# Kernel optimization log

Hardware: AMD Instinct MI355X
Metric: run time of the kernel (lower is better)

The kernel has to match this reference:

```python
import jax, jax.numpy as jnp
import numpy as np

N_NODES = 100000
N_EDGES = 640000
IN_C, HID_C, OUT_C = 128, 256, 128
N_GRAPHS = 64


def setup_inputs() -> dict:
    key = jax.random.key(0)
    k1, k2, k3, k4, k5, k6, k7 = jax.random.split(key, 7)
    x = jax.random.normal(k1, (N_NODES, IN_C), dtype=jnp.float32)
    edge_index = jax.random.randint(k2, (2, N_EDGES), 0, N_NODES, dtype=jnp.int32)
    batch = jnp.sort(jax.random.randint(k3, (N_NODES,), 0, N_GRAPHS, dtype=jnp.int32))
    s1 = 1.0 / np.sqrt(IN_C)
    s2 = 1.0 / np.sqrt(HID_C)
    W1 = jax.random.uniform(k4, (IN_C, HID_C), jnp.float32, -s1, s1)
    b1 = jax.random.uniform(k5, (HID_C,), jnp.float32, -s1, s1)
    W2 = jax.random.uniform(k6, (HID_C, OUT_C), jnp.float32, -s2, s2)
    b2 = jax.random.uniform(k7, (OUT_C,), jnp.float32, -s2, s2)
    return {"x": x, "edge_index": edge_index, "batch": batch,
            "W1": W1, "b1": b1, "W2": W2, "b2": b2}


def gcn_conv(x, src, dst, W, b, n_nodes):
    # GCNConv: D^{-1/2} (A + I) D^{-1/2} X W + b, degrees computed with self-loops
    ones = jnp.ones(src.shape[0], dtype=x.dtype)
    deg = jax.ops.segment_sum(ones, dst, num_segments=n_nodes) + 1.0  # self-loop
    inv_sqrt_deg = jax.lax.rsqrt(deg)
    h = x @ W  # [N, out]
    coef = inv_sqrt_deg[src] * inv_sqrt_deg[dst]  # [E]
    msgs = h[src] * coef[:, None]  # [E, out] -- dominant memory traffic
    agg = jax.ops.segment_sum(msgs, dst, num_segments=n_nodes)
    agg = agg + h * (inv_sqrt_deg * inv_sqrt_deg)[:, None]  # self-loop term
    return agg + b


def reference(x, edge_index, batch, W1, b1, W2, b2):
    n = x.shape[0]
    src, dst = edge_index[0], edge_index[1]
    h = jax.nn.relu(gcn_conv(x, src, dst, W1, b1, n))
    h = jax.nn.relu(gcn_conv(h, src, dst, W2, b2, n))
    # global mean pool over graphs
    sums = jax.ops.segment_sum(h, batch, num_segments=N_GRAPHS)
    counts = jax.ops.segment_sum(jnp.ones(n, dtype=h.dtype), batch, num_segments=N_GRAPHS)
    graph_embed = sums / jnp.maximum(counts, 1.0)[:, None]
    return h, graph_embed
```

## Files before the change

kernel.cpp:

```cpp
#include <hip/hip_runtime.h>

#define N_NODES  100000
#define N_EDGES  640000
#define IN_C     128
#define HID_C    256
#define OUT_C    128
#define N_GRAPHS 64
#define CAP      32

#define NBUK     256
#define NPB      ((N_NODES + NBUK - 1) / NBUK)
#define NSTRIPE  8
#define SCAP     448
#define BPB      (NSTRIPE * SCAP)
#define EPB      4096
#define EBLK     ((N_EDGES + EPB - 1) / EPB)

typedef _Float16 f16;
typedef _Float16 f16x4 __attribute__((ext_vector_type(4)));
typedef _Float16 f16x8 __attribute__((ext_vector_type(8)));
typedef float    f32x4 __attribute__((ext_vector_type(4)));


__global__ void zero_gcur_kernel(int* __restrict__ g) {
    int i = blockIdx.x * 256 + threadIdx.x;
    if (i < NBUK * NSTRIPE) g[i] = 0;
}


__global__ __launch_bounds__(256) void phaseA_kernel(
    const int* __restrict__ src, const int* __restrict__ dst,
    int* __restrict__ gcur, int* __restrict__ buckets,
    const float* __restrict__ x, f16* __restrict__ xh,
    const float* __restrict__ W1, f16* __restrict__ Wt1,
    const float* __restrict__ W2, f16* __restrict__ Wt2,
    int* __restrict__ gs) {
    int b = blockIdx.x;
    if (b < EBLK) {
        __shared__ int bcnt[NBUK];
        __shared__ int bbase[NBUK];
        int tid = threadIdx.x;
        int st  = b & (NSTRIPE - 1);
        for (int i = tid; i < NBUK; i += 256) bcnt[i] = 0;
        __syncthreads();
        int e0 = b * EPB + tid * 16;
        bool act = e0 < N_EDGES;
        int bk[16], pp[16], val[16];
        #pragma unroll
        for (int c = 0; c < 4; ++c) {
            int e = e0 + c * 4;
            int4 dq = act ? *reinterpret_cast<const int4*>(&dst[e]) : make_int4(0,0,0,0);
            int4 sq = act ? *reinterpret_cast<const int4*>(&src[e]) : make_int4(0,0,0,0);
            int dv[4] = {dq.x, dq.y, dq.z, dq.w};
            int sv[4] = {sq.x, sq.y, sq.z, sq.w};
            #pragma unroll
            for (int j = 0; j < 4; ++j) {
                int k = c * 4 + j;
                int bkj = (unsigned)dv[j] / NPB;
                bk[k]  = bkj;
                val[k] = ((dv[j] - bkj * NPB) << 17) | sv[j];
            }
        }
        #pragma unroll
        for (int k = 0; k < 16; ++k)
            pp[k] = act ? atomicAdd(&bcnt[bk[k]], 1) : 0;
        __syncthreads();
        if (tid < NBUK) {
            int c = bcnt[tid];
            if (c > 0) bbase[tid] = atomicAdd(&gcur[tid * NSTRIPE + st], c);
        }
        __syncthreads();
        if (act) {
            #pragma unroll
            for (int k = 0; k < 16; ++k) {
                int idx = bbase[bk[k]] + pp[k];
                if (idx < SCAP)
                    buckets[(size_t)bk[k] * BPB + st * SCAP + idx] = val[k];
            }
        }
        return;
    }
    b -= EBLK;
    if (b < 6250) {
        int i = (b * 256 + threadIdx.x) * 8;
        float4 a = *reinterpret_cast<const float4*>(&x[i]);
        float4 c = *reinterpret_cast<const float4*>(&x[i + 4]);
        f16x8 o = { (f16)a.x, (f16)a.y, (f16)a.z, (f16)a.w,
                    (f16)c.x, (f16)c.y, (f16)c.z, (f16)c.w };
        *reinterpret_cast<f16x8*>(&xh[i]) = o;
        return;
    }
    b -= 6250;
    if (b < 128) {
        int idx = b * 256 + threadIdx.x;
        int k = idx / HID_C, n = idx % HID_C;
        Wt1[n * IN_C + k] = (f16)W1[idx];
        return;
    }
    b -= 128;
    if (b < 128) {
        int idx = b * 256 + threadIdx.x;
        int k = idx / OUT_C, n = idx % OUT_C;
        Wt2[n * HID_C + k] = (f16)W2[idx];
        return;
    }
    if (threadIdx.x <= N_GRAPHS) gs[threadIdx.x] = N_NODES;
}
#define PHASEA_BLOCKS (EBLK + 6250 + 128 + 128 + 1)


__global__ __launch_bounds__(256) void phaseB_kernel(
    const int* __restrict__ gcur, const int* __restrict__ buckets,
    int2* __restrict__ meta, int* __restrict__ slots, float* __restrict__ isd,
    const int* __restrict__ batch, int* __restrict__ gs) {
    int b = blockIdx.x;
    if (b < NBUK) {
        __shared__ int cur[NPB];
        int tid = threadIdx.x;
        int v0 = b * NPB;
        int nv = min(NPB, N_NODES - v0);
        for (int i = tid; i < NPB; i += 256) cur[i] = 0;
        __syncthreads();
        for (int s = 0; s < NSTRIPE; ++s) {
            int n = min(gcur[b * NSTRIPE + s], SCAP);
            const int* seg = &buckets[(size_t)b * BPB + s * SCAP];
            for (int i = tid; i < n; i += 256) {
                int e = seg[i];
                int r = e >> 17;
                int pos = atomicAdd(&cur[r], 1);
                if (pos < CAP) slots[(size_t)(v0 + r) * CAP + pos] = e & 0x1FFFF;
            }
        }
        __syncthreads();
        for (int i = tid; i < nv; i += 256) {
            int c = cur[i];
            float iv = rsqrtf((float)c + 1.0f);
            meta[v0 + i] = make_int2(c, __float_as_int(iv));
            isd[v0 + i] = iv;
        }
        return;
    }
    b -= NBUK;
    int i = b * 256 + threadIdx.x;
    if (i < N_NODES) {
        int bt = batch[i];
        int pb = (i == 0) ? -1 : batch[i - 1];
        for (int g = pb + 1; g <= bt; ++g) gs[g] = i;
    }
}
#define PHASEB_BLOCKS (NBUK + (N_NODES + 255) / 256)


__global__ __launch_bounds__(512, 4) void gemm_fused_kernel(
    const f16* __restrict__ A,
    const f16* __restrict__ Wt1,
    const f16* __restrict__ Wt2,
    const float* __restrict__ b1,
    const float* __restrict__ isd,
    f16* __restrict__ T2, int M) {
    __shared__ f16 Wl[128 * 132];
    __shared__ f16 bounce[8][2][16 * 40];
    int tid  = threadIdx.x;
    int wid  = tid >> 6;
    int lane = tid & 63;
    int l16  = lane & 15;
    int kgrp = lane >> 4;
    int rowbase = blockIdx.x * 128 + wid * 16;
    int arow = rowbase + l16;
    bool okrow = arow < M;

    f16x8 a1[4];
    f16x8 zero = {};
    #pragma unroll
    for (int s = 0; s < 4; ++s)
        a1[s] = okrow ? *reinterpret_cast<const f16x8*>(&A[(size_t)arow * IN_C + s * 32 + kgrp * 8])
                      : zero;

    f16x4 p1[16];
    #pragma unroll
    for (int c = 0; c < 2; ++c) {
        #pragma unroll
        for (int g = 0; g < 4; ++g) {
            int idx = g * 512 + tid;
            int col = idx >> 4;
            int gg  = idx & 15;
            *reinterpret_cast<f16x8*>(&Wl[col * 132 + gg * 8]) =
                *reinterpret_cast<const f16x8*>(&Wt1[(size_t)(c * 128 + col) * IN_C + gg * 8]);
        }
        __syncthreads();
        f32x4 acc1[8] = {};
        #pragma unroll
        for (int t = 0; t < 8; ++t) {
            #pragma unroll
            for (int s = 0; s < 4; ++s) {
                f16x8 b = *reinterpret_cast<const f16x8*>(
                    &Wl[(t * 16 + l16) * 132 + s * 32 + kgrp * 8]);
                acc1[t] = __builtin_amdgcn_mfma_f32_16x16x32_f16(a1[s], b, acc1[t], 0, 0, 0);
            }
        }
        #pragma unroll
        for (int t = 0; t < 8; ++t) {
            float bb = b1[c * 128 + t * 16 + l16];
            #pragma unroll
            for (int j = 0; j < 4; ++j)
                p1[c * 8 + t][j] = (f16)fmaxf(acc1[t][j] + bb, 0.f);
        }
        __syncthreads();
    }
    int crow0 = rowbase + kgrp * 4;
    float sv[4];
    #pragma unroll
    for (int j = 0; j < 4; ++j)
        sv[j] = (crow0 + j < M) ? isd[crow0 + j] : 0.f;

    #pragma unroll
    for (int c2 = 0; c2 < 2; ++c2) {
        #pragma unroll
        for (int g = 0; g < 4; ++g) {
            int idx = g * 512 + tid;
            int col = idx >> 5;
            int gg  = idx & 31;
            *reinterpret_cast<f16x8*>(&Wl[col * 260 + gg * 8]) =
                *reinterpret_cast<const f16x8*>(&Wt2[(size_t)(c2 * 64 + col) * HID_C + gg * 8]);
        }
        __syncthreads();
        f32x4 acc2[4] = {};
        #pragma unroll
        for (int s = 0; s < 8; ++s) {
            f16* buf = &bounce[wid][s & 1][0];
            #pragma unroll
            for (int half = 0; half < 2; ++half) {
                int t = 2 * s + half;
                #pragma unroll
                for (int j = 0; j < 4; ++j)
                    buf[(kgrp * 4 + j) * 40 + half * 16 + l16] = p1[t][j];
            }
            f16x8 a2 = *reinterpret_cast<const f16x8*>(&buf[l16 * 40 + kgrp * 8]);
            #pragma unroll
            for (int ct = 0; ct < 4; ++ct) {
                f16x8 b = *reinterpret_cast<const f16x8*>(
                    &Wl[(ct * 16 + l16) * 260 + s * 32 + kgrp * 8]);
                acc2[ct] = __builtin_amdgcn_mfma_f32_16x16x32_f16(a2, b, acc2[ct], 0, 0, 0);
            }
        }
        #pragma unroll
        for (int ct = 0; ct < 4; ++ct) {
            int col = c2 * 64 + ct * 16 + l16;
            #pragma unroll
            for (int j = 0; j < 4; ++j) {
                int row = crow0 + j;
                if (row < M)
                    T2[(size_t)row * OUT_C + col] = (f16)(acc2[ct][j] * sv[j]);
            }
        }
        __syncthreads();
    }
}


template <bool COEF, bool BIAS_RELU, typename OutT>
__global__ __launch_bounds__(256) void agg_kernel(
    const f16* __restrict__ h, const int2* __restrict__ meta,
    const int* __restrict__ slots, const float* __restrict__ bias,
    OutT* __restrict__ out) {
    constexpr int C = 128;
    int wid  = threadIdx.x >> 6;
    int lane = threadIdx.x & 63;
    int q    = lane >> 4;
    int ln   = lane & 15;
    int vA = blockIdx.x * 8 + wid * 2;
    if (vA >= N_NODES) return;
    int vB = vA + 1;
    bool hasB = vB < N_NODES;
    int baseA = vA * CAP;
    int baseB = hasB ? vB * CAP : 0;

    int2 mA = meta[vA];
    int2 mB = hasB ? meta[vB] : make_int2(0, 0);
    int ra0 = slots[baseA + q];
    int ra1 = slots[baseA + q + 4];
    int rb0 = slots[baseB + q];
    int rb1 = slots[baseB + q + 4];
    f16x8 hvS = {};
    if (q < 2 && (q == 0 || hasB)) {
        int vS = q ? vB : vA;
        hvS = *reinterpret_cast<const f16x8*>(&h[(size_t)vS * C + ln * 8]);
    }

    int ia0 = ((unsigned)ra0 < N_NODES) ? ra0 : 0;
    int ia1 = ((unsigned)ra1 < N_NODES) ? ra1 : 0;
    int ib0 = ((unsigned)rb0 < N_NODES) ? rb0 : 0;
    int ib1 = ((unsigned)rb1 < N_NODES) ? rb1 : 0;

    f16x8 ha0 = *reinterpret_cast<const f16x8*>(&h[(size_t)ia0 * C + ln * 8]);
    f16x8 ha1 = *reinterpret_cast<const f16x8*>(&h[(size_t)ia1 * C + ln * 8]);
    f16x8 hb0 = *reinterpret_cast<const f16x8*>(&h[(size_t)ib0 * C + ln * 8]);
    f16x8 hb1 = *reinterpret_cast<const f16x8*>(&h[(size_t)ib1 * C + ln * 8]);

    int eA = min(mA.x, CAP);
    int eB = hasB ? min(mB.x, CAP) : 0;
    float ivA = __int_as_float(mA.y);
    float ivB = hasB ? __int_as_float(mB.y) : 0.f;

    bool mA0 = q < eA,     mA1 = q + 4 < eA;
    bool mB0 = q < eB,     mB1 = q + 4 < eB;
    f16 ca0, ca1, cb0, cb1;
    if constexpr (COEF) {
        ca0 = (f16)(mA0 ? __int_as_float(meta[ia0].y) * ivA : 0.f);
        ca1 = (f16)(mA1 ? __int_as_float(meta[ia1].y) * ivA : 0.f);
        cb0 = (f16)(mB0 ? __int_as_float(meta[ib0].y) * ivB : 0.f);
        cb1 = (f16)(mB1 ? __int_as_float(meta[ib1].y) * ivB : 0.f);
    } else {
        ca0 = (f16)(mA0 ? 1.f : 0.f);
        ca1 = (f16)(mA1 ? 1.f : 0.f);
        cb0 = (f16)(mB0 ? 1.f : 0.f);
        cb1 = (f16)(mB1 ? 1.f : 0.f);
    }
    f16x8 acc0 = {}, acc1 = {};
    {
        f16x8 va0 = {ca0, ca0, ca0, ca0, ca0, ca0, ca0, ca0};
        f16x8 va1 = {ca1, ca1, ca1, ca1, ca1, ca1, ca1, ca1};
        f16x8 vb0 = {cb0, cb0, cb0, cb0, cb0, cb0, cb0, cb0};
        f16x8 vb1 = {cb1, cb1, cb1, cb1, cb1, cb1, cb1, cb1};
        acc0 += va0 * ha0;
        acc0 += va1 * ha1;
        acc1 += vb0 * hb0;
        acc1 += vb1 * hb1;
    }

    int tA = 8 + q, tB = 8 + q;
    while (__any((tA < eA) || (tB < eB))) {
        bool nA0 = tA < eA, nA1 = tA + 4 < eA;
        bool nB0 = tB < eB, nB1 = tB + 4 < eB;
        int ja0 = slots[baseA + (nA0 ? tA     : 0)];
        int ja1 = slots[baseA + (nA1 ? tA + 4 : 0)];
        int jb0 = slots[baseB + (nB0 ? tB     : 0)];
        int jb1 = slots[baseB + (nB1 ? tB + 4 : 0)];
        ja0 = ((unsigned)ja0 < N_NODES) ? ja0 : 0;
        ja1 = ((unsigned)ja1 < N_NODES) ? ja1 : 0;
        jb0 = ((unsigned)jb0 < N_NODES) ? jb0 : 0;
        jb1 = ((unsigned)jb1 < N_NODES) ? jb1 : 0;
        f16 da0, da1, db0, db1;
        if constexpr (COEF) {
            da0 = (f16)(nA0 ? __int_as_float(meta[ja0].y) * ivA : 0.f);
            da1 = (f16)(nA1 ? __int_as_float(meta[ja1].y) * ivA : 0.f);
            db0 = (f16)(nB0 ? __int_as_float(meta[jb0].y) * ivB : 0.f);
            db1 = (f16)(nB1 ? __int_as_float(meta[jb1].y) * ivB : 0.f);
        } else {
            da0 = (f16)(nA0 ? 1.f : 0.f);
            da1 = (f16)(nA1 ? 1.f : 0.f);
            db0 = (f16)(nB0 ? 1.f : 0.f);
            db1 = (f16)(nB1 ? 1.f : 0.f);
        }
        f16x8 ga0 = *reinterpret_cast<const f16x8*>(&h[(size_t)ja0 * C + ln * 8]);
        f16x8 ga1 = *reinterpret_cast<const f16x8*>(&h[(size_t)ja1 * C + ln * 8]);
        f16x8 gb0 = *reinterpret_cast<const f16x8*>(&h[(size_t)jb0 * C + ln * 8]);
        f16x8 gb1 = *reinterpret_cast<const f16x8*>(&h[(size_t)jb1 * C + ln * 8]);
        f16x8 wa0 = {da0, da0, da0, da0, da0, da0, da0, da0};
        f16x8 wa1 = {da1, da1, da1, da1, da1, da1, da1, da1};
        f16x8 wb0 = {db0, db0, db0, db0, db0, db0, db0, db0};
        f16x8 wb1 = {db1, db1, db1, db1, db1, db1, db1, db1};
        acc0 += wa0 * ga0;
        acc0 += wa1 * ga1;
        acc1 += wb0 * gb0;
        acc1 += wb1 * gb1;
        tA += 8; tB += 8;
    }

    #pragma unroll
    for (int st = 16; st <= 32; st <<= 1) {
        int4 r0 = __builtin_bit_cast(int4, acc0);
        int4 r1 = __builtin_bit_cast(int4, acc1);
        int4 s0, s1;
        s0.x = __shfl_xor(r0.x, st, 64); s0.y = __shfl_xor(r0.y, st, 64);
        s0.z = __shfl_xor(r0.z, st, 64); s0.w = __shfl_xor(r0.w, st, 64);
        s1.x = __shfl_xor(r1.x, st, 64); s1.y = __shfl_xor(r1.y, st, 64);
        s1.z = __shfl_xor(r1.z, st, 64); s1.w = __shfl_xor(r1.w, st, 64);
        acc0 += __builtin_bit_cast(f16x8, s0);
        acc1 += __builtin_bit_cast(f16x8, s1);
    }
    if (q < 2) {
        bool ok = (q == 0) || hasB;
        if (ok) {
            int v = q ? vB : vA;
            float iv = q ? ivB : ivA;
            f16x8 accv = q ? acc1 : acc0;
            float t[8];
            if constexpr (COEF) {
                float cs = iv * iv;
                #pragma unroll
                for (int i = 0; i < 8; ++i) t[i] = (float)accv[i] + cs * (float)hvS[i];
            } else {
                #pragma unroll
                for (int i = 0; i < 8; ++i) t[i] = iv * ((float)accv[i] + (float)hvS[i]);
            }
            if constexpr (BIAS_RELU) {
                float4 b0 = *reinterpret_cast<const float4*>(&bias[ln * 8]);
                float4 b1 = *reinterpret_cast<const float4*>(&bias[ln * 8 + 4]);
                float bb[8] = {b0.x, b0.y, b0.z, b0.w, b1.x, b1.y, b1.z, b1.w};
                float o[8];
                #pragma unroll
                for (int i = 0; i < 8; ++i)
                    o[i] = fmaxf(t[i] + bb[i], 0.f);
                *reinterpret_cast<float4*>(&out[(size_t)v * C + ln * 8]) =
                    make_float4(o[0], o[1], o[2], o[3]);
                *reinterpret_cast<float4*>(&out[(size_t)v * C + ln * 8 + 4]) =
                    make_float4(o[4], o[5], o[6], o[7]);
            } else {
                f16x8 o;
                #pragma unroll
                for (int i = 0; i < 8; ++i) o[i] = (f16)t[i];
                *reinterpret_cast<f16x8*>(&out[(size_t)v * C + ln * 8]) = o;
            }
        }
    }
}


#define POOL_PARTS 16
__global__ void pool_partial_kernel(const float* __restrict__ h, const int* __restrict__ gs,
                                    float* __restrict__ psums) {
    int g    = blockIdx.x >> 4;
    int part = blockIdx.x & 15;
    int ch   = threadIdx.x;
    int s = gs[g], e = gs[g + 1];
    float acc = 0.f;
    for (int i = s + part; i < e; i += POOL_PARTS)
        acc += h[(size_t)i * OUT_C + ch];
    psums[(size_t)(g * POOL_PARTS + part) * OUT_C + ch] = acc;
}

__global__ void pool_final_kernel(const float* __restrict__ psums, const int* __restrict__ gs,
                                  float* __restrict__ out2) {
    int g = blockIdx.x, ch = threadIdx.x;
    float acc = 0.f;
    #pragma unroll
    for (int p = 0; p < POOL_PARTS; ++p)
        acc += psums[(size_t)(g * POOL_PARTS + p) * OUT_C + ch];
    int c = gs[g + 1] - gs[g];
    out2[g * OUT_C + ch] = acc / fmaxf((float)c, 1.0f);
}


extern "C" void kernel_launch(void* const* d_in, const int* in_sizes, int n_in,
                              void* d_out, int out_size, void* d_ws, size_t ws_size,
                              hipStream_t stream) {
    const float* x     = (const float*)d_in[0];
    const int*   ei    = (const int*)d_in[1];
    const int*   src   = ei;
    const int*   dst   = ei + N_EDGES;
    const int*   batch = (const int*)d_in[2];
    const float* W1    = (const float*)d_in[3];
    const float* b1    = (const float*)d_in[4];
    const float* W2    = (const float*)d_in[5];
    const float* b2    = (const float*)d_in[6];

    float* out    = (float*)d_out;
    float* h_out  = out;
    float* ge_out = out + (size_t)N_NODES * OUT_C;

    char* wsp = (char*)d_ws;
    auto alloc = [&](size_t bytes) -> char* {
        char* p = wsp;
        wsp += (bytes + 255) & ~(size_t)255;
        return p;
    };
    int2*  meta    = (int2*)alloc((size_t)N_NODES * 8);
    float* isd     = (float*)alloc((size_t)N_NODES * 4);
    int*   slots   = (int*)alloc((size_t)N_NODES * CAP * 4);
    int*   gcur    = (int*)alloc((size_t)NBUK * NSTRIPE * 4);
    int*   buckets = (int*)alloc((size_t)NBUK * BPB * 4);
    int*   gs      = (int*)alloc((size_t)(N_GRAPHS + 1) * 4);
    float* psums   = (float*)alloc((size_t)N_GRAPHS * POOL_PARTS * OUT_C * 4);
    f16*   xh      = (f16*)alloc((size_t)N_NODES * IN_C * 2);
    f16*   ax      = (f16*)alloc((size_t)N_NODES * IN_C * 2);
    f16*   t2      = (f16*)alloc((size_t)N_NODES * OUT_C * 2);
    f16*   Wt1     = (f16*)alloc((size_t)IN_C * HID_C * 2);
    f16*   Wt2     = (f16*)alloc((size_t)HID_C * OUT_C * 2);

    zero_gcur_kernel<<<(NBUK * NSTRIPE + 255) / 256, 256, 0, stream>>>(gcur);

    phaseA_kernel<<<PHASEA_BLOCKS, 256, 0, stream>>>(src, dst, gcur, buckets, x, xh,
                                                     W1, Wt1, W2, Wt2, gs);
    phaseB_kernel<<<PHASEB_BLOCKS, 256, 0, stream>>>(gcur, buckets, meta, slots, isd,
                                                     batch, gs);

    agg_kernel<true, false, f16><<<(N_NODES + 7) / 8, 256, 0, stream>>>(
        xh, meta, slots, nullptr, ax);

    gemm_fused_kernel<<<(N_NODES + 127) / 128, 512, 0, stream>>>(
        ax, Wt1, Wt2, b1, isd, t2, N_NODES);

    agg_kernel<false, true, float><<<(N_NODES + 7) / 8, 256, 0, stream>>>(
        t2, meta, slots, b2, h_out);

    pool_partial_kernel<<<N_GRAPHS * POOL_PARTS, OUT_C, 0, stream>>>(h_out, gs, psums);
    pool_final_kernel<<<N_GRAPHS, OUT_C, 0, stream>>>(psums, gs, ge_out);
}
```

Measured before the change: 171.7 us.

## Fuse first-layer neighbor aggregation into the fused GEMM kernel via LDS staging

The standalone first-layer aggregation kernel is folded into the GEMM kernel, now called megafused_kernel. Each wave gathers and normalizes the neighbor sums for its 16 rows. It writes them to a per-wave LDS tile, which then feeds the MFMA GEMM directly, so the intermediate aggregated-feature array no longer makes a round trip through HBM and one launch is dropped. The LDS tile is also reused as the bounce buffer for the second GEMM. In exchange, each wave now processes its 8 node pairs one after another. The larger LDS footprint may also lower occupancy, which could leave the latency-bound gather less hidden than in the separate high-occupancy kernel.

```diff
diff --git a/kernel.cpp b/kernel.cpp
--- a/kernel.cpp
+++ b/kernel.cpp
@@ -151,30 +151,136 @@
 #define PHASEB_BLOCKS (NBUK + (N_NODES + 255) / 256)
 
 
-__global__ __launch_bounds__(512, 4) void gemm_fused_kernel(
-    const f16* __restrict__ A,
+__global__ __launch_bounds__(512, 4) void megafused_kernel(
+    const f16* __restrict__ xh, const int2* __restrict__ meta,
+    const int* __restrict__ slots,
     const f16* __restrict__ Wt1,
     const f16* __restrict__ Wt2,
     const float* __restrict__ b1,
     const float* __restrict__ isd,
     f16* __restrict__ T2, int M) {
+    constexpr int C = 128;
     __shared__ f16 Wl[128 * 132];
-    __shared__ f16 bounce[8][2][16 * 40];
+    __shared__ f16 axs[8][16 * 136];
     int tid  = threadIdx.x;
     int wid  = tid >> 6;
     int lane = tid & 63;
     int l16  = lane & 15;
     int kgrp = lane >> 4;
+    int q    = kgrp;
+    int ln   = l16;
     int rowbase = blockIdx.x * 128 + wid * 16;
-    int arow = rowbase + l16;
-    bool okrow = arow < M;
+
+    for (int pair = 0; pair < 8; ++pair) {
+        int vA = rowbase + pair * 2;
+        if (vA >= M) break;
+        int vB = vA + 1;
+        bool hasB = vB < M;
+        int baseA = vA * CAP;
+        int baseB = hasB ? vB * CAP : 0;
+
+        int2 mA = meta[vA];
+        int2 mB = hasB ? meta[vB] : make_int2(0, 0);
+        int ra0 = slots[baseA + q];
+        int ra1 = slots[baseA + q + 4];
+        int rb0 = slots[baseB + q];
+        int rb1 = slots[baseB + q + 4];
+        f16x8 hvS = {};
+        if (q < 2 && (q == 0 || hasB)) {
+            int vS = q ? vB : vA;
+            hvS = *reinterpret_cast<const f16x8*>(&xh[(size_t)vS * C + ln * 8]);
+        }
+        int ia0 = ((unsigned)ra0 < N_NODES) ? ra0 : 0;
+        int ia1 = ((unsigned)ra1 < N_NODES) ? ra1 : 0;
+        int ib0 = ((unsigned)rb0 < N_NODES) ? rb0 : 0;
+        int ib1 = ((unsigned)rb1 < N_NODES) ? rb1 : 0;
+
+        f16x8 ha0 = *reinterpret_cast<const f16x8*>(&xh[(size_t)ia0 * C + ln * 8]);
+        f16x8 ha1 = *reinterpret_cast<const f16x8*>(&xh[(size_t)ia1 * C + ln * 8]);
+        f16x8 hb0 = *reinterpret_cast<const f16x8*>(&xh[(size_t)ib0 * C + ln * 8]);
+        f16x8 hb1 = *reinterpret_cast<const f16x8*>(&xh[(size_t)ib1 * C + ln * 8]);
+
+        int eA = min(mA.x, CAP);
+        int eB = hasB ? min(mB.x, CAP) : 0;
+        float ivA = __int_as_float(mA.y);
+        float ivB = hasB ? __int_as_float(mB.y) : 0.f;
+
+        bool mA0 = q < eA,     mA1 = q + 4 < eA;
+        bool mB0 = q < eB,     mB1 = q + 4 < eB;
+        f16 ca0 = (f16)(mA0 ? __int_as_float(meta[ia0].y) * ivA : 0.f);
+        f16 ca1 = (f16)(mA1 ? __int_as_float(meta[ia1].y) * ivA : 0.f);
+        f16 cb0 = (f16)(mB0 ? __int_as_float(meta[ib0].y) * ivB : 0.f);
+        f16 cb1 = (f16)(mB1 ? __int_as_float(meta[ib1].y) * ivB : 0.f);
+
+        f16x8 acc0 = {}, acc1 = {};
+        {
+            f16x8 va0 = {ca0, ca0, ca0, ca0, ca0, ca0, ca0, ca0};
+            f16x8 va1 = {ca1, ca1, ca1, ca1, ca1, ca1, ca1, ca1};
+            f16x8 vb0 = {cb0, cb0, cb0, cb0, cb0, cb0, cb0, cb0};
+            f16x8 vb1 = {cb1, cb1, cb1, cb1, cb1, cb1, cb1, cb1};
+            acc0 += va0 * ha0;
+            acc0 += va1 * ha1;
+            acc1 += vb0 * hb0;
+            acc1 += vb1 * hb1;
+        }
+        int tA = 8 + q, tB = 8 + q;
+        while (__any((tA < eA) || (tB < eB))) {
+            bool nA0 = tA < eA, nA1 = tA + 4 < eA;
+            bool nB0 = tB < eB, nB1 = tB + 4 < eB;
+            int ja0 = slots[baseA + (nA0 ? tA     : 0)];
+            int ja1 = slots[baseA + (nA1 ? tA + 4 : 0)];
+            int jb0 = slots[baseB + (nB0 ? tB     : 0)];
+            int jb1 = slots[baseB + (nB1 ? tB + 4 : 0)];
+            ja0 = ((unsigned)ja0 < N_NODES) ? ja0 : 0;
+            ja1 = ((unsigned)ja1 < N_NODES) ? ja1 : 0;
+            jb0 = ((unsigned)jb0 < N_NODES) ? jb0 : 0;
+            jb1 = ((unsigned)jb1 < N_NODES) ? jb1 : 0;
+            f16 da0 = (f16)(nA0 ? __int_as_float(meta[ja0].y) * ivA : 0.f);
+            f16 da1 = (f16)(nA1 ? __int_as_float(meta[ja1].y) * ivA : 0.f);
+            f16 db0 = (f16)(nB0 ? __int_as_float(meta[jb0].y) * ivB : 0.f);
+            f16 db1 = (f16)(nB1 ? __int_as_float(meta[jb1].y) * ivB : 0.f);
+            f16x8 ga0 = *reinterpret_cast<const f16x8*>(&xh[(size_t)ja0 * C + ln * 8]);
+            f16x8 ga1 = *reinterpret_cast<const f16x8*>(&xh[(size_t)ja1 * C + ln * 8]);
+            f16x8 gb0 = *reinterpret_cast<const f16x8*>(&xh[(size_t)jb0 * C + ln * 8]);
+            f16x8 gb1 = *reinterpret_cast<const f16x8*>(&xh[(size_t)jb1 * C + ln * 8]);
+            f16x8 wa0 = {da0, da0, da0, da0, da0, da0, da0, da0};
+            f16x8 wa1 = {da1, da1, da1, da1, da1, da1, da1, da1};
+            f16x8 wb0 = {db0, db0, db0, db0, db0, db0, db0, db0};
+            f16x8 wb1 = {db1, db1, db1, db1, db1, db1, db1, db1};
+            acc0 += wa0 * ga0;
+            acc0 += wa1 * ga1;
+            acc1 += wb0 * gb0;
+            acc1 += wb1 * gb1;
+            tA += 8; tB += 8;
+        }
+        #pragma unroll
+        for (int st = 16; st <= 32; st <<= 1) {
+            int4 r0 = __builtin_bit_cast(int4, acc0);
+            int4 r1 = __builtin_bit_cast(int4, acc1);
+            int4 s0, s1;
+            s0.x = __shfl_xor(r0.x, st, 64); s0.y = __shfl_xor(r0.y, st, 64);
+            s0.z = __shfl_xor(r0.z, st, 64); s0.w = __shfl_xor(r0.w, st, 64);
+            s1.x = __shfl_xor(r1.x, st, 64); s1.y = __shfl_xor(r1.y, st, 64);
+            s1.z = __shfl_xor(r1.z, st, 64); s1.w = __shfl_xor(r1.w, st, 64);
+            acc0 += __builtin_bit_cast(f16x8, s0);
+            acc1 += __builtin_bit_cast(f16x8, s1);
+        }
+        if (q < 2 && (q == 0 || hasB)) {
+            float iv = q ? ivB : ivA;
+            f16x8 accv = q ? acc1 : acc0;
+            float cs = iv * iv;
+            f16x8 o;
+            #pragma unroll
+            for (int i = 0; i < 8; ++i)
+                o[i] = (f16)((float)accv[i] + cs * (float)hvS[i]);
+            *reinterpret_cast<f16x8*>(&axs[wid][(pair * 2 + q) * 136 + ln * 8]) = o;
+        }
+    }
 
     f16x8 a1[4];
-    f16x8 zero = {};
     #pragma unroll
     for (int s = 0; s < 4; ++s)
-        a1[s] = okrow ? *reinterpret_cast<const f16x8*>(&A[(size_t)arow * IN_C + s * 32 + kgrp * 8])
-                      : zero;
+        a1[s] = *reinterpret_cast<const f16x8*>(&axs[wid][l16 * 136 + s * 32 + kgrp * 8]);
 
     f16x4 p1[16];
     #pragma unroll
@@ -188,14 +294,14 @@
                 *reinterpret_cast<const f16x8*>(&Wt1[(size_t)(c * 128 + col) * IN_C + gg * 8]);
         }
         __syncthreads();
-        f32x4 acc1[8] = {};
+        f32x4 acc1r[8] = {};
         #pragma unroll
         for (int t = 0; t < 8; ++t) {
             #pragma unroll
             for (int s = 0; s < 4; ++s) {
                 f16x8 b = *reinterpret_cast<const f16x8*>(
                     &Wl[(t * 16 + l16) * 132 + s * 32 + kgrp * 8]);
-                acc1[t] = __builtin_amdgcn_mfma_f32_16x16x32_f16(a1[s], b, acc1[t], 0, 0, 0);
+                acc1r[t] = __builtin_amdgcn_mfma_f32_16x16x32_f16(a1[s], b, acc1r[t], 0, 0, 0);
             }
         }
         #pragma unroll
@@ -203,7 +309,7 @@
             float bb = b1[c * 128 + t * 16 + l16];
             #pragma unroll
             for (int j = 0; j < 4; ++j)
-                p1[c * 8 + t][j] = (f16)fmaxf(acc1[t][j] + bb, 0.f);
+                p1[c * 8 + t][j] = (f16)fmaxf(acc1r[t][j] + bb, 0.f);
         }
         __syncthreads();
     }
@@ -227,7 +333,7 @@
         f32x4 acc2[4] = {};
         #pragma unroll
         for (int s = 0; s < 8; ++s) {
-            f16* buf = &bounce[wid][s & 1][0];
+            f16* buf = &axs[wid][(s & 1) * 680];
             #pragma unroll
             for (int half = 0; half < 2; ++half) {
                 int t = 2 * s + half;
@@ -258,11 +364,10 @@
 }
 
 
-template <bool COEF, bool BIAS_RELU, typename OutT>
-__global__ __launch_bounds__(256) void agg_kernel(
+__global__ __launch_bounds__(256) void agg2_kernel(
     const f16* __restrict__ h, const int2* __restrict__ meta,
     const int* __restrict__ slots, const float* __restrict__ bias,
-    OutT* __restrict__ out) {
+    float* __restrict__ out) {
     constexpr int C = 128;
     int wid  = threadIdx.x >> 6;
     int lane = threadIdx.x & 63;
@@ -302,20 +407,10 @@
     float ivA = __int_as_float(mA.y);
     float ivB = hasB ? __int_as_float(mB.y) : 0.f;
 
-    bool mA0 = q < eA,     mA1 = q + 4 < eA;
-    bool mB0 = q < eB,     mB1 = q + 4 < eB;
-    f16 ca0, ca1, cb0, cb1;
-    if constexpr (COEF) {
-        ca0 = (f16)(mA0 ? __int_as_float(meta[ia0].y) * ivA : 0.f);
-        ca1 = (f16)(mA1 ? __int_as_float(meta[ia1].y) * ivA : 0.f);
-        cb0 = (f16)(mB0 ? __int_as_float(meta[ib0].y) * ivB : 0.f);
-        cb1 = (f16)(mB1 ? __int_as_float(meta[ib1].y) * ivB : 0.f);
-    } else {
-        ca0 = (f16)(mA0 ? 1.f : 0.f);
-        ca1 = (f16)(mA1 ? 1.f : 0.f);
-        cb0 = (f16)(mB0 ? 1.f : 0.f);
-        cb1 = (f16)(mB1 ? 1.f : 0.f);
-    }
+    f16 ca0 = (f16)((q < eA)     ? 1.f : 0.f);
+    f16 ca1 = (f16)((q + 4 < eA) ? 1.f : 0.f);
+    f16 cb0 = (f16)((q < eB)     ? 1.f : 0.f);
+    f16 cb1 = (f16)((q + 4 < eB) ? 1.f : 0.f);
     f16x8 acc0 = {}, acc1 = {};
     {
         f16x8 va0 = {ca0, ca0, ca0, ca0, ca0, ca0, ca0, ca0};
@@ -340,18 +435,10 @@
         ja1 = ((unsigned)ja1 < N_NODES) ? ja1 : 0;
         jb0 = ((unsigned)jb0 < N_NODES) ? jb0 : 0;
         jb1 = ((unsigned)jb1 < N_NODES) ? jb1 : 0;
-        f16 da0, da1, db0, db1;
-        if constexpr (COEF) {
-            da0 = (f16)(nA0 ? __int_as_float(meta[ja0].y) * ivA : 0.f);
-            da1 = (f16)(nA1 ? __int_as_float(meta[ja1].y) * ivA : 0.f);
-            db0 = (f16)(nB0 ? __int_as_float(meta[jb0].y) * ivB : 0.f);
-            db1 = (f16)(nB1 ? __int_as_float(meta[jb1].y) * ivB : 0.f);
-        } else {
-            da0 = (f16)(nA0 ? 1.f : 0.f);
-            da1 = (f16)(nA1 ? 1.f : 0.f);
-            db0 = (f16)(nB0 ? 1.f : 0.f);
-            db1 = (f16)(nB1 ? 1.f : 0.f);
-        }
+        f16 da0 = (f16)(nA0 ? 1.f : 0.f);
+        f16 da1 = (f16)(nA1 ? 1.f : 0.f);
+        f16 db0 = (f16)(nB0 ? 1.f : 0.f);
+        f16 db1 = (f16)(nB1 ? 1.f : 0.f);
         f16x8 ga0 = *reinterpret_cast<const f16x8*>(&h[(size_t)ja0 * C + ln * 8]);
         f16x8 ga1 = *reinterpret_cast<const f16x8*>(&h[(size_t)ja1 * C + ln * 8]);
         f16x8 gb0 = *reinterpret_cast<const f16x8*>(&h[(size_t)jb0 * C + ln * 8]);
@@ -385,33 +472,17 @@
             int v = q ? vB : vA;
             float iv = q ? ivB : ivA;
             f16x8 accv = q ? acc1 : acc0;
-            float t[8];
-            if constexpr (COEF) {
-                float cs = iv * iv;
-                #pragma unroll
-                for (int i = 0; i < 8; ++i) t[i] = (float)accv[i] + cs * (float)hvS[i];
-            } else {
-                #pragma unroll
-                for (int i = 0; i < 8; ++i) t[i] = iv * ((float)accv[i] + (float)hvS[i]);
-            }
-            if constexpr (BIAS_RELU) {
-                float4 b0 = *reinterpret_cast<const float4*>(&bias[ln * 8]);
-                float4 b1 = *reinterpret_cast<const float4*>(&bias[ln * 8 + 4]);
-                float bb[8] = {b0.x, b0.y, b0.z, b0.w, b1.x, b1.y, b1.z, b1.w};
-                float o[8];
-                #pragma unroll
-                for (int i = 0; i < 8; ++i)
-                    o[i] = fmaxf(t[i] + bb[i], 0.f);
-                *reinterpret_cast<float4*>(&out[(size_t)v * C + ln * 8]) =
-                    make_float4(o[0], o[1], o[2], o[3]);
-                *reinterpret_cast<float4*>(&out[(size_t)v * C + ln * 8 + 4]) =
-                    make_float4(o[4], o[5], o[6], o[7]);
-            } else {
-                f16x8 o;
-                #pragma unroll
-                for (int i = 0; i < 8; ++i) o[i] = (f16)t[i];
-                *reinterpret_cast<f16x8*>(&out[(size_t)v * C + ln * 8]) = o;
-            }
+            float4 b0 = *reinterpret_cast<const float4*>(&bias[ln * 8]);
+            float4 b1v = *reinterpret_cast<const float4*>(&bias[ln * 8 + 4]);
+            float bb[8] = {b0.x, b0.y, b0.z, b0.w, b1v.x, b1v.y, b1v.z, b1v.w};
+            float o[8];
+            #pragma unroll
+            for (int i = 0; i < 8; ++i)
+                o[i] = fmaxf(iv * ((float)accv[i] + (float)hvS[i]) + bb[i], 0.f);
+            *reinterpret_cast<float4*>(&out[(size_t)v * C + ln * 8]) =
+                make_float4(o[0], o[1], o[2], o[3]);
+            *reinterpret_cast<float4*>(&out[(size_t)v * C + ln * 8 + 4]) =
+                make_float4(o[4], o[5], o[6], o[7]);
         }
     }
 }
@@ -473,7 +544,6 @@
     int*   gs      = (int*)alloc((size_t)(N_GRAPHS + 1) * 4);
     float* psums   = (float*)alloc((size_t)N_GRAPHS * POOL_PARTS * OUT_C * 4);
     f16*   xh      = (f16*)alloc((size_t)N_NODES * IN_C * 2);
-    f16*   ax      = (f16*)alloc((size_t)N_NODES * IN_C * 2);
     f16*   t2      = (f16*)alloc((size_t)N_NODES * OUT_C * 2);
     f16*   Wt1     = (f16*)alloc((size_t)IN_C * HID_C * 2);
     f16*   Wt2     = (f16*)alloc((size_t)HID_C * OUT_C * 2);
@@ -485,14 +555,10 @@
     phaseB_kernel<<<PHASEB_BLOCKS, 256, 0, stream>>>(gcur, buckets, meta, slots, isd,
                                                      batch, gs);
 
-    agg_kernel<true, false, f16><<<(N_NODES + 7) / 8, 256, 0, stream>>>(
-        xh, meta, slots, nullptr, ax);
-
-    gemm_fused_kernel<<<(N_NODES + 127) / 128, 512, 0, stream>>>(
-        ax, Wt1, Wt2, b1, isd, t2, N_NODES);
-
-    agg_kernel<false, true, float><<<(N_NODES + 7) / 8, 256, 0, stream>>>(
-        t2, meta, slots, b2, h_out);
+    megafused_kernel<<<(N_NODES + 127) / 128, 512, 0, stream>>>(
+        xh, meta, slots, Wt1, Wt2, b1, isd, t2, N_NODES);
+
+    agg2_kernel<<<(N_NODES + 7) / 8, 256, 0, stream>>>(t2, meta, slots, b2, h_out);
 
     pool_partial_kernel<<<N_GRAPHS * POOL_PARTS, OUT_C, 0, stream>>>(h_out, gs, psums);
     pool_final_kernel<<<N_GRAPHS, OUT_C, 0, stream>>>(psums, gs, ge_out);
```

Result: slower. 180.0 us (+4.9%).
